# Kernel tuning notes

Hardware: AMD Instinct MI355X
Metric: run time of the kernel (lower is better)

Reference implementation:

```python
import jax, jax.numpy as jnp
import numpy as np
from jax import lax

WINDOW_SIZE = 11
SIGMA = 1.5
MAX_VAL = 1.0


def _gaussian_kernel_2d(window_size: int, sigma: float) -> jnp.ndarray:
    coords = jnp.arange(window_size, dtype=jnp.float32) - window_size // 2
    g = jnp.exp(-coords ** 2 / (2.0 * sigma ** 2))
    g = g / g.sum()
    k2d = jnp.outer(g, g)
    return k2d / k2d.sum()  # [W, W]


def _depthwise_conv(x: jnp.ndarray, k2d: jnp.ndarray) -> jnp.ndarray:
    # x: [B, C, H, W]; depthwise (groups=C) conv with SAME padding
    C = x.shape[1]
    ws = k2d.shape[0]
    kernel = jnp.broadcast_to(k2d[None, None], (C, 1, ws, ws)).astype(x.dtype)  # [C,1,ws,ws]
    pad = ws // 2
    return lax.conv_general_dilated(
        x, kernel,
        window_strides=(1, 1),
        padding=((pad, pad), (pad, pad)),
        dimension_numbers=('NCHW', 'OIHW', 'NCHW'),
        feature_group_count=C,
    )


def setup_inputs() -> dict:
    key = jax.random.key(0)
    k1, k2 = jax.random.split(key)
    B, C, H, W = 16, 3, 512, 512
    sr = jax.random.uniform(k1, (B, C, H, W), dtype=jnp.float32)
    hr = jax.random.uniform(k2, (B, C, H, W), dtype=jnp.float32)
    return {"sr": sr, "hr": hr}


def reference(sr, hr):
    c1 = (0.01 * MAX_VAL) ** 2
    c2 = (0.03 * MAX_VAL) ** 2
    k2d = _gaussian_kernel_2d(WINDOW_SIZE, SIGMA)

    mu1 = _depthwise_conv(sr, k2d)
    mu2 = _depthwise_conv(hr, k2d)
    mu1_sq = mu1 ** 2
    mu2_sq = mu2 ** 2
    mu1_mu2 = mu1 * mu2
    sigma1_sq = _depthwise_conv(sr * sr, k2d) - mu1_sq
    sigma2_sq = _depthwise_conv(hr * hr, k2d) - mu2_sq
    sigma12 = _depthwise_conv(sr * hr, k2d) - mu1_mu2

    ssim_map = (2 * mu1_mu2 + c1) * (2 * sigma12 + c2) / (
        (mu1_sq + mu2_sq + c1) * (sigma1_sq + sigma2_sq + c2) + 1e-12)
    return 1.0 - ssim_map.mean()
```

## Files before the change

### kernel.cpp

```cpp
#include <hip/hip_runtime.h>


typedef __attribute__((ext_vector_type(2))) float  f32x2;
typedef __attribute__((ext_vector_type(4))) float  f32x4;
typedef __fp16 f16;
typedef __attribute__((ext_vector_type(2))) __fp16 h2v;
typedef __attribute__((ext_vector_type(4))) __fp16 h4;
typedef __attribute__((ext_vector_type(8))) __fp16 h8;

constexpr int IMG_H = 512;
constexpr int IMG_W = 512;
constexpr int NBC   = 48;
constexpr int TW    = 64;
constexpr int TH    = 32;
constexpr int NBLKX = IMG_W / TW;
constexpr int NBLKY = IMG_H / TH;
constexpr int NBLK  = NBLKX * NBLKY * NBC;

constexpr int XP   = 104;
constexpr int XR   = 48;
constexpr int XQS  = XR * XP;
constexpr int HTP  = 72;
constexpr int HTQS = 64 * HTP;
constexpr int SMEMH = 5 * XQS;
static_assert(5 * HTQS <= SMEMH, "Ht must fit in X union");

constexpr float C1 = 1.0e-4f;
constexpr float C2 = 9.0e-4f;

__device__ const float GW[11] = {
    0.00102838f, 0.00759876f, 0.03600077f, 0.10936070f, 0.21300553f,
    0.26601172f, 0.21300553f, 0.10936070f, 0.03600077f, 0.00759876f,
    0.00102838f};

__device__ __forceinline__ h8 ldfrag(const f16* __restrict__ gtab, int base) {
    h8 b;
#pragma unroll
    for (int i = 0; i < 8; ++i) b[i] = gtab[base + i];
    return b;
}

__global__ __launch_bounds__(64) void ssim_init(double* acc) {
    if (threadIdx.x == 0) acc[0] = 0.0;
}

__global__ __launch_bounds__(256, 3) void ssim_main(const float* __restrict__ sr,
                                                    const float* __restrict__ hr,
                                                    double* __restrict__ sink,
                                                    int mode) {
    __shared__ __align__(16) f16 smem[SMEMH];
    __shared__ __align__(8)  f16 gtab[128];
    __shared__ float wsums[4];

    const int tid  = threadIdx.x;
    const int w    = tid >> 6;
    const int lane = tid & 63;
    const int l15  = lane & 15;
    const int grp8 = (lane >> 4) << 3;
    const int grp4 = (lane >> 4) << 2;

    const int bc  = blockIdx.z;
    const int gr0 = blockIdx.y * TH - 5;
    const int gc0 = blockIdx.x * TW - 8;
    const float* __restrict__ srp = sr + (size_t)bc * IMG_H * IMG_W;
    const float* __restrict__ hrp = hr + (size_t)bc * IMG_H * IMG_W;

    const int c8  = tid & 15;
    const int r0s = tid >> 4;
    float4 La0[3], La1[3], Lb0[3], Lb1[3];
#pragma unroll
    for (int t = 0; t < 3; ++t) {
        const int r  = r0s + 16 * t;
        const int gr = gr0 + r;
        const int gc = gc0 + c8 * 8;
        La0[t] = La1[t] = Lb0[t] = Lb1[t] = (float4){0.f, 0.f, 0.f, 0.f};
        if ((c8 < 13) & (r < 42) &
            ((unsigned)gr < (unsigned)IMG_H) & ((unsigned)gc < (unsigned)IMG_W)) {
            const float4* pa = (const float4*)&srp[(size_t)gr * IMG_W + gc];
            const float4* pb = (const float4*)&hrp[(size_t)gr * IMG_W + gc];
            La0[t] = pa[0]; La1[t] = pa[1];
            Lb0[t] = pb[0]; Lb1[t] = pb[1];
        }
    }

    if (tid < 128) {
        const int d = tid - 66;
        float v = 0.f;
        if ((unsigned)d <= 10u) v = GW[d];
        gtab[tid] = (f16)v;
    }

    if (c8 < 13) {
#pragma unroll
        for (int t = 0; t < 3; ++t) {
            const int r = r0s + 16 * t;
            const f32x2* a0 = (const f32x2*)&La0[t];
            const f32x2* a1 = (const f32x2*)&La1[t];
            const f32x2* b0 = (const f32x2*)&Lb0[t];
            const f32x2* b1 = (const f32x2*)&Lb1[t];
            const f32x2 aa0 = a0[0] * a0[0], aa1 = a0[1] * a0[1];
            const f32x2 aa2 = a1[0] * a1[0], aa3 = a1[1] * a1[1];
            const f32x2 bb0 = b0[0] * b0[0], bb1 = b0[1] * b0[1];
            const f32x2 bb2 = b1[0] * b1[0], bb3 = b1[1] * b1[1];
            const f32x2 ab0 = a0[0] * b0[0], ab1 = a0[1] * b0[1];
            const f32x2 ab2 = a1[0] * b1[0], ab3 = a1[1] * b1[1];
            union { h2v h2[4]; h8 v; } uva, uvb, uaa, ubb, uab;
            uva.h2[0] = __builtin_amdgcn_cvt_pkrtz(a0[0].x, a0[0].y);
            uva.h2[1] = __builtin_amdgcn_cvt_pkrtz(a0[1].x, a0[1].y);
            uva.h2[2] = __builtin_amdgcn_cvt_pkrtz(a1[0].x, a1[0].y);
            uva.h2[3] = __builtin_amdgcn_cvt_pkrtz(a1[1].x, a1[1].y);
            uvb.h2[0] = __builtin_amdgcn_cvt_pkrtz(b0[0].x, b0[0].y);
            uvb.h2[1] = __builtin_amdgcn_cvt_pkrtz(b0[1].x, b0[1].y);
            uvb.h2[2] = __builtin_amdgcn_cvt_pkrtz(b1[0].x, b1[0].y);
            uvb.h2[3] = __builtin_amdgcn_cvt_pkrtz(b1[1].x, b1[1].y);
            uaa.h2[0] = __builtin_amdgcn_cvt_pkrtz(aa0.x, aa0.y);
            uaa.h2[1] = __builtin_amdgcn_cvt_pkrtz(aa1.x, aa1.y);
            uaa.h2[2] = __builtin_amdgcn_cvt_pkrtz(aa2.x, aa2.y);
            uaa.h2[3] = __builtin_amdgcn_cvt_pkrtz(aa3.x, aa3.y);
            ubb.h2[0] = __builtin_amdgcn_cvt_pkrtz(bb0.x, bb0.y);
            ubb.h2[1] = __builtin_amdgcn_cvt_pkrtz(bb1.x, bb1.y);
            ubb.h2[2] = __builtin_amdgcn_cvt_pkrtz(bb2.x, bb2.y);
            ubb.h2[3] = __builtin_amdgcn_cvt_pkrtz(bb3.x, bb3.y);
            uab.h2[0] = __builtin_amdgcn_cvt_pkrtz(ab0.x, ab0.y);
            uab.h2[1] = __builtin_amdgcn_cvt_pkrtz(ab1.x, ab1.y);
            uab.h2[2] = __builtin_amdgcn_cvt_pkrtz(ab2.x, ab2.y);
            uab.h2[3] = __builtin_amdgcn_cvt_pkrtz(ab3.x, ab3.y);
            const int o = r * XP + c8 * 8;
            *(h8*)&smem[0 * XQS + o] = uva.v;
            *(h8*)&smem[1 * XQS + o] = uvb.v;
            *(h8*)&smem[2 * XQS + o] = uaa.v;
            *(h8*)&smem[3 * XQS + o] = ubb.v;
            *(h8*)&smem[4 * XQS + o] = uab.v;
        }
    }
    __syncthreads();

    float s16 = 0.f;
#pragma unroll
    for (int d = 0; d <= 10; ++d) s16 += (float)gtab[66 + d];
    const float rs = 1.0f / (s16 * s16);

    const int ksb = (w >= 2) ? 1 : 0;
    const int nks = (w & 1) ? 2 : 1;
    const int bhb = 66 + ksb * 32 + grp8 - (16 * w + l15 + 3);
    const h8 bh0 = ldfrag(gtab, bhb);
    h8 bh1 = {};
    if (nks == 2) bh1 = ldfrag(gtab, bhb + 32);

    f32x4 acc[5][3] = {};
#pragma unroll
    for (int Mt = 0; Mt < 3; ++Mt) {
        const int arow = (16 * Mt + l15) * XP + grp8;
#pragma unroll
        for (int q = 0; q < 5; ++q) {
            const h8 af = *(const h8*)&smem[q * XQS + arow + ksb * 32];
            acc[q][Mt] = __builtin_amdgcn_mfma_f32_16x16x32_f16(af, bh0, acc[q][Mt], 0, 0, 0);
        }
        if (nks == 2) {
#pragma unroll
            for (int q = 0; q < 5; ++q) {
                const h8 af = *(const h8*)&smem[q * XQS + arow + ksb * 32 + 32];
                acc[q][Mt] = __builtin_amdgcn_mfma_f32_16x16x32_f16(af, bh1, acc[q][Mt], 0, 0, 0);
            }
        }
    }
    __syncthreads();

#pragma unroll
    for (int q = 0; q < 5; ++q) {
#pragma unroll
        for (int Mt = 0; Mt < 3; ++Mt) {
            union { h2v h2[2]; h4 v; } u;
            u.h2[0] = __builtin_amdgcn_cvt_pkrtz(acc[q][Mt][0], acc[q][Mt][1]);
            u.h2[1] = __builtin_amdgcn_cvt_pkrtz(acc[q][Mt][2], acc[q][Mt][3]);
            *(h4*)&smem[q * HTQS + (16 * w + l15) * HTP + 16 * Mt + grp4] = u.v;
        }
    }

    const h8 bv0 = ldfrag(gtab, 66 + grp8 - l15);
    const h8 bv1 = ldfrag(gtab, 66 + grp8 - 16 - l15);
    const h8 bv2 = ldfrag(gtab, 66 + 32 + grp8 - 16 - l15);
    f32x4 acc2[5][2] = {};
    const int abase = (16 * w + l15) * HTP + grp8;
#pragma unroll
    for (int q = 0; q < 5; ++q) {
        const h8 a0 = *(const h8*)&smem[q * HTQS + abase];
        const h8 a1 = *(const h8*)&smem[q * HTQS + abase + 32];
        acc2[q][0] = __builtin_amdgcn_mfma_f32_16x16x32_f16(a0, bv0, acc2[q][0], 0, 0, 0);
        acc2[q][1] = __builtin_amdgcn_mfma_f32_16x16x32_f16(a0, bv1, acc2[q][1], 0, 0, 0);
        acc2[q][1] = __builtin_amdgcn_mfma_f32_16x16x32_f16(a1, bv2, acc2[q][1], 0, 0, 0);
    }

    float local = 0.f;
#pragma unroll
    for (int nt = 0; nt < 2; ++nt) {
        const f32x4 m1 = acc2[0][nt] * rs;
        const f32x4 m2 = acc2[1][nt] * rs;
        const f32x4 q1 = acc2[2][nt] * rs;
        const f32x4 q2 = acc2[3][nt] * rs;
        const f32x4 pp = acc2[4][nt] * rs;
        const f32x4 mu1s = m1 * m1, mu2s = m2 * m2, mu12 = m1 * m2;
        const f32x4 sg1 = q1 - mu1s, sg2 = q2 - mu2s, sg12 = pp - mu12;
        const f32x4 num = (2.f * mu12 + C1) * (2.f * sg12 + C2);
        const f32x4 den = (mu1s + mu2s + C1) * (sg1 + sg2 + C2) + 1e-12f;
#pragma unroll
        for (int e = 0; e < 4; ++e)
            local += num[e] * __builtin_amdgcn_rcpf(den[e]);
    }

#pragma unroll
    for (int off = 32; off > 0; off >>= 1)
        local += __shfl_down(local, off, 64);
    if ((tid & 63) == 0) wsums[tid >> 6] = local;
    __syncthreads();
    if (tid == 0) {
        const double bsum = (double)(wsums[0] + wsums[1] + wsums[2] + wsums[3]);
        if (mode == 0) {
            const int bid = (blockIdx.z * NBLKY + blockIdx.y) * NBLKX + blockIdx.x;
            sink[bid] = bsum;
        } else {
            atomicAdd(sink, bsum);
        }
    }
}

__global__ __launch_bounds__(256) void ssim_finalize(const double* __restrict__ partial,
                                                     float* __restrict__ out, int count) {
    __shared__ double ws[4];
    double s = 0.0;
    for (int i = threadIdx.x; i < count; i += 256) s += partial[i];
#pragma unroll
    for (int off = 32; off > 0; off >>= 1)
        s += __shfl_down(s, off, 64);
    const int lane = threadIdx.x & 63, wave = threadIdx.x >> 6;
    if (lane == 0) ws[wave] = s;
    __syncthreads();
    if (threadIdx.x == 0) {
        const double tot = ws[0] + ws[1] + ws[2] + ws[3];
        const double n = (double)NBC * IMG_H * IMG_W;
        out[0] = (float)(1.0 - tot / n);
    }
}

extern "C" void kernel_launch(void* const* d_in, const int* in_sizes, int n_in,
                              void* d_out, int out_size, void* d_ws, size_t ws_size,
                              hipStream_t stream) {
    const float* sr = (const float*)d_in[0];
    const float* hr = (const float*)d_in[1];
    float* out = (float*)d_out;
    const dim3 grid(NBLKX, NBLKY, NBC);

    if (ws_size >= (size_t)NBLK * sizeof(double)) {
        double* partial = (double*)d_ws;
        ssim_main<<<grid, dim3(256), 0, stream>>>(sr, hr, partial, 0);
        ssim_finalize<<<dim3(1), dim3(256), 0, stream>>>(partial, out, NBLK);
    } else {
        double* acc = (double*)d_ws;
        ssim_init<<<dim3(1), dim3(64), 0, stream>>>(acc);
        ssim_main<<<grid, dim3(256), 0, stream>>>(sr, hr, acc, 1);
        ssim_finalize<<<dim3(1), dim3(256), 0, stream>>>(acc, out, 1);
    }
}
```

Before: 148.2 us.

## Merge squared-sum planes and restructure banded MFMA convolution to fewer passes

Because the SSIM formula only needs sigma1^2 + sigma2^2, the separate sr^2 and hr^2 planes are merged into one plane, so four filtered planes are used instead of five. The horizontal MFMA pass is reorganised so each wave handles a 16-column slice with a single K=32 band fragment, and the vertical pass uses two MFMAs per plane instead of three. The staged input width shrinks to 80 columns and LDS shrinks, so launch bounds are raised to allow 4 blocks per CU. The risk is extra fp16 precision loss from summing the squares before conversion, and tile and band-index bookkeeping errors in the new fragment offsets.

```diff
diff --git a/kernel.cpp b/kernel.cpp
--- a/kernel.cpp
+++ b/kernel.cpp
@@ -22,8 +22,8 @@
 constexpr int XQS  = XR * XP;
 constexpr int HTP  = 72;
 constexpr int HTQS = 64 * HTP;
-constexpr int SMEMH = 5 * XQS;
-static_assert(5 * HTQS <= SMEMH, "Ht must fit in X union");
+constexpr int SMEMH = 4 * XQS;
+static_assert(4 * HTQS <= SMEMH, "Ht must fit in X union");
 
 constexpr float C1 = 1.0e-4f;
 constexpr float C2 = 9.0e-4f;
@@ -44,7 +44,7 @@
     if (threadIdx.x == 0) acc[0] = 0.0;
 }
 
-__global__ __launch_bounds__(256, 3) void ssim_main(const float* __restrict__ sr,
+__global__ __launch_bounds__(256, 4) void ssim_main(const float* __restrict__ sr,
                                                     const float* __restrict__ hr,
                                                     double* __restrict__ sink,
                                                     int mode) {
@@ -74,7 +74,7 @@
         const int gr = gr0 + r;
         const int gc = gc0 + c8 * 8;
         La0[t] = La1[t] = Lb0[t] = Lb1[t] = (float4){0.f, 0.f, 0.f, 0.f};
-        if ((c8 < 13) & (r < 42) &
+        if ((c8 < 10) & (r < 42) &
             ((unsigned)gr < (unsigned)IMG_H) & ((unsigned)gc < (unsigned)IMG_W)) {
             const float4* pa = (const float4*)&srp[(size_t)gr * IMG_W + gc];
             const float4* pb = (const float4*)&hrp[(size_t)gr * IMG_W + gc];
@@ -90,7 +90,7 @@
         gtab[tid] = (f16)v;
     }
 
-    if (c8 < 13) {
+    if (c8 < 10) {
 #pragma unroll
         for (int t = 0; t < 3; ++t) {
             const int r = r0s + 16 * t;
@@ -98,13 +98,13 @@
             const f32x2* a1 = (const f32x2*)&La1[t];
             const f32x2* b0 = (const f32x2*)&Lb0[t];
             const f32x2* b1 = (const f32x2*)&Lb1[t];
-            const f32x2 aa0 = a0[0] * a0[0], aa1 = a0[1] * a0[1];
-            const f32x2 aa2 = a1[0] * a1[0], aa3 = a1[1] * a1[1];
-            const f32x2 bb0 = b0[0] * b0[0], bb1 = b0[1] * b0[1];
-            const f32x2 bb2 = b1[0] * b1[0], bb3 = b1[1] * b1[1];
-            const f32x2 ab0 = a0[0] * b0[0], ab1 = a0[1] * b0[1];
-            const f32x2 ab2 = a1[0] * b1[0], ab3 = a1[1] * b1[1];
-            union { h2v h2[4]; h8 v; } uva, uvb, uaa, ubb, uab;
+            const f32x2 s0 = a0[0] * a0[0] + b0[0] * b0[0];
+            const f32x2 s1 = a0[1] * a0[1] + b0[1] * b0[1];
+            const f32x2 s2 = a1[0] * a1[0] + b1[0] * b1[0];
+            const f32x2 s3 = a1[1] * a1[1] + b1[1] * b1[1];
+            const f32x2 p0 = a0[0] * b0[0], p1 = a0[1] * b0[1];
+            const f32x2 p2 = a1[0] * b1[0], p3 = a1[1] * b1[1];
+            union { h2v h2[4]; h8 v; } uva, uvb, uss, uab;
             uva.h2[0] = __builtin_amdgcn_cvt_pkrtz(a0[0].x, a0[0].y);
             uva.h2[1] = __builtin_amdgcn_cvt_pkrtz(a0[1].x, a0[1].y);
             uva.h2[2] = __builtin_amdgcn_cvt_pkrtz(a1[0].x, a1[0].y);
@@ -113,24 +113,19 @@
             uvb.h2[1] = __builtin_amdgcn_cvt_pkrtz(b0[1].x, b0[1].y);
             uvb.h2[2] = __builtin_amdgcn_cvt_pkrtz(b1[0].x, b1[0].y);
             uvb.h2[3] = __builtin_amdgcn_cvt_pkrtz(b1[1].x, b1[1].y);
-            uaa.h2[0] = __builtin_amdgcn_cvt_pkrtz(aa0.x, aa0.y);
-            uaa.h2[1] = __builtin_amdgcn_cvt_pkrtz(aa1.x, aa1.y);
-            uaa.h2[2] = __builtin_amdgcn_cvt_pkrtz(aa2.x, aa2.y);
-            uaa.h2[3] = __builtin_amdgcn_cvt_pkrtz(aa3.x, aa3.y);
-            ubb.h2[0] = __builtin_amdgcn_cvt_pkrtz(bb0.x, bb0.y);
-            ubb.h2[1] = __builtin_amdgcn_cvt_pkrtz(bb1.x, bb1.y);
-            ubb.h2[2] = __builtin_amdgcn_cvt_pkrtz(bb2.x, bb2.y);
-            ubb.h2[3] = __builtin_amdgcn_cvt_pkrtz(bb3.x, bb3.y);
-            uab.h2[0] = __builtin_amdgcn_cvt_pkrtz(ab0.x, ab0.y);
-            uab.h2[1] = __builtin_amdgcn_cvt_pkrtz(ab1.x, ab1.y);
-            uab.h2[2] = __builtin_amdgcn_cvt_pkrtz(ab2.x, ab2.y);
-            uab.h2[3] = __builtin_amdgcn_cvt_pkrtz(ab3.x, ab3.y);
+            uss.h2[0] = __builtin_amdgcn_cvt_pkrtz(s0.x, s0.y);
+            uss.h2[1] = __builtin_amdgcn_cvt_pkrtz(s1.x, s1.y);
+            uss.h2[2] = __builtin_amdgcn_cvt_pkrtz(s2.x, s2.y);
+            uss.h2[3] = __builtin_amdgcn_cvt_pkrtz(s3.x, s3.y);
+            uab.h2[0] = __builtin_amdgcn_cvt_pkrtz(p0.x, p0.y);
+            uab.h2[1] = __builtin_amdgcn_cvt_pkrtz(p1.x, p1.y);
+            uab.h2[2] = __builtin_amdgcn_cvt_pkrtz(p2.x, p2.y);
+            uab.h2[3] = __builtin_amdgcn_cvt_pkrtz(p3.x, p3.y);
             const int o = r * XP + c8 * 8;
             *(h8*)&smem[0 * XQS + o] = uva.v;
             *(h8*)&smem[1 * XQS + o] = uvb.v;
-            *(h8*)&smem[2 * XQS + o] = uaa.v;
-            *(h8*)&smem[3 * XQS + o] = ubb.v;
-            *(h8*)&smem[4 * XQS + o] = uab.v;
+            *(h8*)&smem[2 * XQS + o] = uss.v;
+            *(h8*)&smem[3 * XQS + o] = uab.v;
         }
     }
     __syncthreads();
@@ -140,34 +135,21 @@
     for (int d = 0; d <= 10; ++d) s16 += (float)gtab[66 + d];
     const float rs = 1.0f / (s16 * s16);
 
-    const int ksb = (w >= 2) ? 1 : 0;
-    const int nks = (w & 1) ? 2 : 1;
-    const int bhb = 66 + ksb * 32 + grp8 - (16 * w + l15 + 3);
-    const h8 bh0 = ldfrag(gtab, bhb);
-    h8 bh1 = {};
-    if (nks == 2) bh1 = ldfrag(gtab, bhb + 32);
-
-    f32x4 acc[5][3] = {};
+    const h8 bh = ldfrag(gtab, 63 + grp8 - l15);
+    f32x4 acc[4][3] = {};
 #pragma unroll
     for (int Mt = 0; Mt < 3; ++Mt) {
-        const int arow = (16 * Mt + l15) * XP + grp8;
-#pragma unroll
-        for (int q = 0; q < 5; ++q) {
-            const h8 af = *(const h8*)&smem[q * XQS + arow + ksb * 32];
-            acc[q][Mt] = __builtin_amdgcn_mfma_f32_16x16x32_f16(af, bh0, acc[q][Mt], 0, 0, 0);
-        }
-        if (nks == 2) {
-#pragma unroll
-            for (int q = 0; q < 5; ++q) {
-                const h8 af = *(const h8*)&smem[q * XQS + arow + ksb * 32 + 32];
-                acc[q][Mt] = __builtin_amdgcn_mfma_f32_16x16x32_f16(af, bh1, acc[q][Mt], 0, 0, 0);
-            }
-        }
-    }
-    __syncthreads();
-
-#pragma unroll
-    for (int q = 0; q < 5; ++q) {
+        const int arow = (16 * Mt + l15) * XP + 16 * w + grp8;
+#pragma unroll
+        for (int q = 0; q < 4; ++q) {
+            const h8 af = *(const h8*)&smem[q * XQS + arow];
+            acc[q][Mt] = __builtin_amdgcn_mfma_f32_16x16x32_f16(af, bh, acc[q][Mt], 0, 0, 0);
+        }
+    }
+    __syncthreads();
+
+#pragma unroll
+    for (int q = 0; q < 4; ++q) {
 #pragma unroll
         for (int Mt = 0; Mt < 3; ++Mt) {
             union { h2v h2[2]; h4 v; } u;
@@ -177,18 +159,15 @@
         }
     }
 
-    const h8 bv0 = ldfrag(gtab, 66 + grp8 - l15);
-    const h8 bv1 = ldfrag(gtab, 66 + grp8 - 16 - l15);
-    const h8 bv2 = ldfrag(gtab, 66 + 32 + grp8 - 16 - l15);
-    f32x4 acc2[5][2] = {};
+    const h8 bv = ldfrag(gtab, 66 + grp8 - l15);
+    f32x4 acc2[4][2] = {};
     const int abase = (16 * w + l15) * HTP + grp8;
 #pragma unroll
-    for (int q = 0; q < 5; ++q) {
+    for (int q = 0; q < 4; ++q) {
         const h8 a0 = *(const h8*)&smem[q * HTQS + abase];
-        const h8 a1 = *(const h8*)&smem[q * HTQS + abase + 32];
-        acc2[q][0] = __builtin_amdgcn_mfma_f32_16x16x32_f16(a0, bv0, acc2[q][0], 0, 0, 0);
-        acc2[q][1] = __builtin_amdgcn_mfma_f32_16x16x32_f16(a0, bv1, acc2[q][1], 0, 0, 0);
-        acc2[q][1] = __builtin_amdgcn_mfma_f32_16x16x32_f16(a1, bv2, acc2[q][1], 0, 0, 0);
+        const h8 a1 = *(const h8*)&smem[q * HTQS + abase + 16];
+        acc2[q][0] = __builtin_amdgcn_mfma_f32_16x16x32_f16(a0, bv, acc2[q][0], 0, 0, 0);
+        acc2[q][1] = __builtin_amdgcn_mfma_f32_16x16x32_f16(a1, bv, acc2[q][1], 0, 0, 0);
     }
 
     float local = 0.f;
@@ -196,13 +175,13 @@
     for (int nt = 0; nt < 2; ++nt) {
         const f32x4 m1 = acc2[0][nt] * rs;
         const f32x4 m2 = acc2[1][nt] * rs;
-        const f32x4 q1 = acc2[2][nt] * rs;
-        const f32x4 q2 = acc2[3][nt] * rs;
-        const f32x4 pp = acc2[4][nt] * rs;
+        const f32x4 S  = acc2[2][nt] * rs;
+        const f32x4 pp = acc2[3][nt] * rs;
         const f32x4 mu1s = m1 * m1, mu2s = m2 * m2, mu12 = m1 * m2;
-        const f32x4 sg1 = q1 - mu1s, sg2 = q2 - mu2s, sg12 = pp - mu12;
+        const f32x4 sg12 = pp - mu12;
+        const f32x4 sgs  = S - mu1s - mu2s;
         const f32x4 num = (2.f * mu12 + C1) * (2.f * sg12 + C2);
-        const f32x4 den = (mu1s + mu2s + C1) * (sg1 + sg2 + C2) + 1e-12f;
+        const f32x4 den = (mu1s + mu2s + C1) * (sgs + C2) + 1e-12f;
 #pragma unroll
         for (int e = 0; e < 4; ++e)
             local += num[e] * __builtin_amdgcn_rcpf(den[e]);
```

Measured after the change: 133.9 us. 9.7% less time.
